# Optimization experiments

Measured on AMD Instinct MI355X. Metric: run time of the kernel, lower is better.

Reference implementation:

```python
import jax, jax.numpy as jnp
import numpy as np

N5, N4, N3, K = 10242, 2562, 642, 7  # icosphere node counts (levels 5,4,3), spatial kernel size
M = 32  # mchannel
EPS = 1e-8


def _sconv(x, neigh, W, b, relu=True):
    # x: [B,T,N,Cin]; neigh: [N,K] 1-ring indices; W: [K,Cin,Cout]
    xn = x[:, :, neigh, :]                        # [B,T,N,K,Cin] irregular gather
    y = jnp.einsum('btnkc,kcd->btnd', xn, W) + b  # per-node kernel contraction
    return jax.nn.relu(y) if relu else y


def _spool(x, pidx):
    # max-pool fine->coarse mesh: pidx [Ncoarse,Kp] indexes fine nodes
    return jnp.max(x[:, :, pidx, :], axis=3)


def _unpool(x, uidx):
    # coarse->fine copy: uidx [Nfine] indexes coarse nodes
    return x[:, :, uidx, :]


def _cos(f, a):
    # torch.nn.CosineSimilarity(dim=-1): dot / max(|f|*|a|, eps)
    dot = jnp.sum(f * a, axis=-1)
    nf = jnp.linalg.norm(f, axis=-1)
    na = jnp.linalg.norm(a, axis=-1)
    return dot / jnp.maximum(nf * na, EPS)


def setup_inputs() -> dict:
    key = jax.random.key(0)
    ks = jax.random.split(key, 32)
    w = lambda i, shape: jax.random.normal(ks[i], shape, jnp.float32) * 0.05
    inp = {
        'frame': jax.random.normal(ks[0], (1, 16, N5, 3), jnp.float32),
        'aem': jax.random.normal(ks[1], (1, 16, N5), jnp.float32),
        'W0f': w(2, (K, 3, M)),        'b0f': w(3, (M,)),
        'W0a': w(4, (K, 1, M)),        'b0a': w(5, (M,)),
        'W1f': w(6, (K, M, 2 * M)),    'b1f': w(7, (2 * M,)),
        'W1a': w(8, (K, M, 2 * M)),    'b1a': w(9, (2 * M,)),
        'W2f': w(10, (K, 2 * M, 4 * M)), 'b2f': w(11, (4 * M,)),
        'W2a': w(12, (K, 2 * M, 4 * M)), 'b2a': w(13, (4 * M,)),
        'W7': w(14, (K, 12 * M, 2 * M)), 'b7': w(15, (2 * M,)),
        'W8': w(16, (K, 4 * M, M)),    'b8': w(17, (M,)),
        'W9': w(18, (K, M, 1)),        'b9': w(19, (1,)),
        'neigh5': jax.random.randint(ks[20], (N5, K), 0, N5),
        'neigh4': jax.random.randint(ks[21], (N4, K), 0, N4),
        'neigh3': jax.random.randint(ks[22], (N3, K), 0, N3),
        'pool5': jax.random.randint(ks[23], (N4, K), 0, N5),
        'pool4': jax.random.randint(ks[24], (N3, K), 0, N4),
        'up4': jax.random.randint(ks[25], (N4,), 0, N3),
        'up5': jax.random.randint(ks[26], (N5,), 0, N4),
        'Tlocation': jax.random.randint(ks[27], (1, 16), 0, 16),
    }
    return inp


def reference(frame, aem, W0f, b0f, W0a, b0a, W1f, b1f, W1a, b1a, W2f, b2f,
              W2a, b2a, W7, b7, W8, b8, W9, b9,
              neigh5, neigh4, neigh3, pool5, pool4, up4, up5, Tlocation):
    a = aem[..., None]                                    # [B,T,N5,1]
    # encoder level 0 (N5)
    c0f = _sconv(frame, neigh5, W0f, b0f)
    c0a = _sconv(a, neigh5, W0a, b0a)
    p0f = _spool(c0f, pool5)
    p0a = _spool(c0a, pool5)
    m0 = _cos(c0f, c0a)[..., None]                        # [B,T,N5,1]
    c0f_att, c0a_att = c0f * m0, c0a * m0
    # encoder level 1 (N4)
    c1f = _sconv(p0f, neigh4, W1f, b1f)
    c1a = _sconv(p0a, neigh4, W1a, b1a)
    p1f = _spool(c1f, pool4)
    p1a = _spool(c1a, pool4)
    m1 = _cos(c1f, c1a)[..., None]
    c1f_att, c1a_att = c1f * m1, c1a * m1
    # bottleneck (N3)
    c2f = _sconv(p1f, neigh3, W2f, b2f)
    c2a = _sconv(p1a, neigh3, W2a, b2a)
    m2 = _cos(c2f, c2a)[..., None]
    conv2 = jnp.concatenate((c2f * m2, c2a * m2), axis=-1)  # [B,T,N3,8M]
    # decoder
    cat7 = jnp.concatenate((_unpool(conv2, up4), c1f_att, c1a_att), axis=-1)  # [B,T,N4,12M]
    conv7 = _sconv(cat7, neigh4, W7, b7)
    cat8 = jnp.concatenate((_unpool(conv7, up5), c0f_att, c0a_att), axis=-1)  # [B,T,N5,4M]
    conv8 = _sconv(cat8, neigh5, W8, b8)
    conv9 = _sconv(conv8, neigh5, W9, b9, relu=False)[..., 0]  # [B,T,N5]
    return jax.nn.softmax(conv9, axis=-1)
```

## Files before the change

### kernel.cpp

```cpp
#include <hip/hip_runtime.h>
#include <cfloat>
#include <cstdint>


constexpr int T  = 16;
constexpr int n5 = 10242, n4 = 2562, n3 = 642;
constexpr int K  = 7;

using bf16x8 = __attribute__((ext_vector_type(8))) short;
using f32x4  = __attribute__((ext_vector_type(4))) float;

static __device__ __forceinline__ float bf2f(unsigned short u) {
    return __uint_as_float((unsigned)u << 16);
}
static __device__ __forceinline__ unsigned short f2bf(float x) {
    unsigned u = __float_as_uint(x);
    u += 0x7FFF + ((u >> 16) & 1);
    return (unsigned short)(u >> 16);
}

__global__ __launch_bounds__(256) void conv0_kernel(
    const float* __restrict__ frame, const float* __restrict__ aem,
    const float* __restrict__ W0f, const float* __restrict__ b0f,
    const float* __restrict__ W0a, const float* __restrict__ b0a,
    const int* __restrict__ neigh5,
    unsigned short* __restrict__ c0f, unsigned short* __restrict__ c0a,
    unsigned short* __restrict__ att0)
{
    const int g = threadIdx.x >> 5;
    const int d = threadIdx.x & 31;
    const int per_t = (n5 + 7) / 8;
    const int t = blockIdx.x / per_t;
    const int n = (blockIdx.x % per_t) * 8 + g;
    if (n >= n5) return;

    float accf = b0f[d];
    float acca = b0a[d];
    const int* nb = neigh5 + n * K;
    #pragma unroll
    for (int k = 0; k < K; ++k) {
        const int j = nb[k];
        const float* fr = frame + ((size_t)t * n5 + j) * 3;
        const float av = aem[(size_t)t * n5 + j];
        accf = fmaf(fr[0], W0f[(k * 3 + 0) * 32 + d], accf);
        accf = fmaf(fr[1], W0f[(k * 3 + 1) * 32 + d], accf);
        accf = fmaf(fr[2], W0f[(k * 3 + 2) * 32 + d], accf);
        acca = fmaf(av, W0a[k * 32 + d], acca);
    }
    accf = fmaxf(accf, 0.f);
    acca = fmaxf(acca, 0.f);

    float dot = accf * acca, ff = accf * accf, aa = acca * acca;
    #pragma unroll
    for (int m = 1; m < 32; m <<= 1) {
        dot += __shfl_xor(dot, m, 32);
        ff  += __shfl_xor(ff,  m, 32);
        aa  += __shfl_xor(aa,  m, 32);
    }
    const float mm = dot / fmaxf(sqrtf(ff) * sqrtf(aa), 1e-8f);
    const size_t base = ((size_t)t * n5 + n) * 32;
    c0f[base + d] = f2bf(accf);
    c0a[base + d] = f2bf(acca);
    const size_t abase = ((size_t)t * n5 + n) * 64;
    att0[abase + d]      = f2bf(accf * mm);
    att0[abase + 32 + d] = f2bf(acca * mm);
}

template<int C>
__global__ __launch_bounds__(256) void pool_kernel(
    const unsigned short* __restrict__ in, const int* __restrict__ pidx,
    int Nin, int Nout, unsigned short* __restrict__ out)
{
    constexpr int C8 = C / 8;
    const int idx = blockIdx.x * 256 + threadIdx.x;
    if (idx >= T * Nout * C8) return;
    const int c8 = idx % C8;
    const int n  = (idx / C8) % Nout;
    const int t  = idx / (C8 * Nout);
    const int* pp = pidx + n * K;
    float m[8];
    #pragma unroll
    for (int j = 0; j < 8; ++j) m[j] = -FLT_MAX;
    #pragma unroll
    for (int k = 0; k < K; ++k) {
        const uint4 v = reinterpret_cast<const uint4*>(in)[((size_t)t * Nin + pp[k]) * C8 + c8];
        const unsigned short* s = reinterpret_cast<const unsigned short*>(&v);
        #pragma unroll
        for (int j = 0; j < 8; ++j) m[j] = fmaxf(m[j], bf2f(s[j]));
    }
    unsigned short o[8];
    #pragma unroll
    for (int j = 0; j < 8; ++j) o[j] = f2bf(m[j]);
    reinterpret_cast<uint4*>(out)[((size_t)t * Nout + n) * C8 + c8] =
        *reinterpret_cast<const uint4*>(o);
}

template<int C, int NN>
__global__ __launch_bounds__(256) void cosatt_kernel(
    const unsigned short* __restrict__ f, const unsigned short* __restrict__ a,
    unsigned short* __restrict__ att)
{
    constexpr int CPL = C / 64;
    const int w = threadIdx.x >> 6, lane = threadIdx.x & 63;
    const int idx = blockIdx.x * 4 + w;
    if (idx >= T * NN) return;
    const unsigned short* fr = f + (size_t)idx * C;
    const unsigned short* ar = a + (size_t)idx * C;
    float xs[CPL], ys[CPL];
    float dot = 0.f, ff = 0.f, aa = 0.f;
    #pragma unroll
    for (int i = 0; i < CPL; ++i) {
        const float x = bf2f(fr[lane + i * 64]);
        const float y = bf2f(ar[lane + i * 64]);
        xs[i] = x; ys[i] = y;
        dot = fmaf(x, y, dot);
        ff  = fmaf(x, x, ff);
        aa  = fmaf(y, y, aa);
    }
    #pragma unroll
    for (int msk = 1; msk < 64; msk <<= 1) {
        dot += __shfl_xor(dot, msk);
        ff  += __shfl_xor(ff,  msk);
        aa  += __shfl_xor(aa,  msk);
    }
    const float m = dot / fmaxf(sqrtf(ff) * sqrtf(aa), 1e-8f);
    unsigned short* orow = att + (size_t)idx * 2 * C;
    #pragma unroll
    for (int i = 0; i < CPL; ++i) {
        orow[lane + i * 64]     = f2bf(xs[i] * m);
        orow[C + lane + i * 64] = f2bf(ys[i] * m);
    }
}

struct PlainB16 {
    const uint4* x; int N; int C8;
    struct Ref { int o; };
    __device__ __forceinline__ Ref prep(int t, int node) const {
        return { (int)(((size_t)t * N + node) * C8) };
    }
    __device__ __forceinline__ uint4 chunk(const Ref& r, int c8) const {
        return x[r.o + c8];
    }
};

struct Cat7B16 {
    const uint4* att2; const uint4* att1; const int* up4;
    __device__ __forceinline__ uint4 row8(int t, int node, int c8) const {
        if (c8 < 32)
            return att2[((size_t)t * n3 + up4[node]) * 32 + c8];
        return att1[((size_t)t * n4 + node) * 16 + (c8 - 32)];
    }
};

struct Cat8B16 {
    const uint4* cv7; const uint4* att0; const int* up5;
    __device__ __forceinline__ uint4 row8(int t, int node, int c8) const {
        if (c8 < 8)
            return cv7[((size_t)t * n4 + up5[node]) * 8 + c8];
        return att0[((size_t)t * n5 + node) * 8 + (c8 - 8)];
    }
};

__global__ __launch_bounds__(256) void wprep_all_kernel(
    const float* __restrict__ W1f, const float* __restrict__ W1a,
    const float* __restrict__ W2f, const float* __restrict__ W2a,
    const float* __restrict__ W7,  const float* __restrict__ W8,
    unsigned short* __restrict__ Wt1f, unsigned short* __restrict__ Wt1a,
    unsigned short* __restrict__ Wt2f, unsigned short* __restrict__ Wt2a,
    unsigned short* __restrict__ Wt7,  unsigned short* __restrict__ Wt8)
{
    int idx = blockIdx.x * 256 + threadIdx.x;
    const float* W; unsigned short* Wt; int KCv, CO;
    if (idx < 14336)       { W = W1f; Wt = Wt1f; KCv = 224;  CO = 64;  }
    else if (idx < 28672)  { idx -= 14336;  W = W1a; Wt = Wt1a; KCv = 224;  CO = 64;  }
    else if (idx < 86016)  { idx -= 28672;  W = W2f; Wt = Wt2f; KCv = 448;  CO = 128; }
    else if (idx < 143360) { idx -= 86016;  W = W2a; Wt = Wt2a; KCv = 448;  CO = 128; }
    else if (idx < 315392) { idx -= 143360; W = W7;  Wt = Wt7;  KCv = 2688; CO = 64;  }
    else                   { idx -= 315392; W = W8;  Wt = Wt8;  KCv = 896;  CO = 32;  }
    const int d = idx / KCv, kc = idx - d * KCv;
    Wt[idx] = f2bf(W[(size_t)kc * CO + d]);
}

template<int CIN, int COUT, int BM, int BN, class Loader>
__global__ __launch_bounds__(256) void gemm_z_kernel(
    Loader ldr, int N, int Mt,
    const unsigned short* __restrict__ Wt,
    unsigned short* __restrict__ Z)
{
    constexpr int KC   = K * CIN;
    constexpr int ND   = K * COUT;
    constexpr int BK   = 64;
    constexpr int KSTEPS = CIN / BK;
    constexpr int U4R  = BK / 8;
    constexpr int WGR_N = BN / 32;
    constexpr int WGR_M = 4 / WGR_N;
    constexpr int DG   = COUT / BN;
    constexpr int NT   = K * DG;
    constexpr int VPTA = BM * U4R / 256;
    constexpr int VPTW = BN * U4R / 256 > 0 ? BN * U4R / 256 : 1;
    static_assert(BM == WGR_M * 32 && CIN % BK == 0 && BN * U4R >= 256);

    __shared__ __align__(16) unsigned short As[BM * BK];
    __shared__ __align__(16) unsigned short Ws[BN * BK];

    const int xcd = blockIdx.x & 7;
    int rest = blockIdx.x >> 3;
    const int half = Mt * NT;
    const int hi = (rest >= half) ? 1 : 0;
    const int t  = 2 * xcd + hi;
    const int j  = rest - hi * half;
    const int tile_m = j / NT;
    const int tnk    = j % NT;
    const int kk_ = tnk / DG;
    const int dg  = tnk % DG;

    const int tid = threadIdx.x, lane = tid & 63, wave = tid >> 6;
    const int wr = wave / WGR_N, wc = wave % WGR_N;
    const int l15 = lane & 15, lhi = lane >> 4;
    const int m0 = tile_m * BM;

    f32x4 acc[2][2] = {};

    for (int ks = 0; ks < KSTEPS; ++ks) {
        uint4 av[VPTA];
        #pragma unroll
        for (int v = 0; v < VPTA; ++v) {
            const int g = tid + v * 256, row = g / U4R, c8 = g % U4R;
            av[v] = ldr.row8(t, min(m0 + row, N - 1), ks * U4R + c8);
        }
        uint4 wv[VPTW];
        #pragma unroll
        for (int v = 0; v < VPTW; ++v) {
            const int g = tid + v * 256, d = g / U4R, c8 = g % U4R;
            wv[v] = *reinterpret_cast<const uint4*>(
                Wt + (size_t)(dg * BN + d) * KC + kk_ * CIN + ks * BK + c8 * 8);
        }

        __syncthreads();
        #pragma unroll
        for (int v = 0; v < VPTA; ++v) {
            const int g = tid + v * 256, row = g / U4R, c8 = g % U4R;
            *reinterpret_cast<uint4*>(&As[(row * BK + c8 * 8) ^ ((row & 7) << 3)]) = av[v];
        }
        #pragma unroll
        for (int v = 0; v < VPTW; ++v) {
            const int g = tid + v * 256, d = g / U4R, c8 = g % U4R;
            *reinterpret_cast<uint4*>(&Ws[(d * BK + c8 * 8) ^ ((d & 7) << 3)]) = wv[v];
        }
        __syncthreads();

        #pragma unroll
        for (int kk2 = 0; kk2 < BK / 32; ++kk2) {
            const int kb = kk2 * 32 + lhi * 8;
            bf16x8 a[2], b[2];
            #pragma unroll
            for (int m = 0; m < 2; ++m) {
                const int row = wr * 32 + m * 16 + l15;
                a[m] = *reinterpret_cast<const bf16x8*>(&As[(row * BK + kb) ^ ((row & 7) << 3)]);
            }
            #pragma unroll
            for (int n = 0; n < 2; ++n) {
                const int col = wc * 32 + n * 16 + l15;
                b[n] = *reinterpret_cast<const bf16x8*>(&Ws[(col * BK + kb) ^ ((col & 7) << 3)]);
            }
            #pragma unroll
            for (int m = 0; m < 2; ++m)
                #pragma unroll
                for (int n = 0; n < 2; ++n)
                    acc[m][n] = __builtin_amdgcn_mfma_f32_16x16x32_bf16(a[m], b[n], acc[m][n], 0, 0, 0);
        }
    }

    const int zc0 = kk_ * COUT + dg * BN;
    #pragma unroll
    for (int n = 0; n < 2; ++n) {
        const int gcol = zc0 + wc * 32 + n * 16 + l15;
        #pragma unroll
        for (int m = 0; m < 2; ++m) {
            #pragma unroll
            for (int i = 0; i < 4; ++i) {
                const int grow = m0 + wr * 32 + m * 16 + lhi * 4 + i;
                if (grow < N)
                    Z[((size_t)t * N + grow) * ND + gcol] = f2bf(acc[m][n][i]);
            }
        }
    }
}

template<int COUT>
__global__ __launch_bounds__(256) void epi_reduce_kernel(
    const unsigned short* __restrict__ Z, const int* __restrict__ neigh, int N,
    const float* __restrict__ bias, unsigned short* __restrict__ out)
{
    constexpr int ND = K * COUT;
    constexpr int C8 = COUT / 8;
    const int idx = blockIdx.x * 256 + threadIdx.x;
    if (idx >= T * N * C8) return;
    const int c8 = idx % C8;
    const int n  = (idx / C8) % N;
    const int t  = idx / (C8 * N);
    const int* nb = neigh + n * K;

    float s[8];
    #pragma unroll
    for (int j = 0; j < 8; ++j) s[j] = bias[c8 * 8 + j];
    #pragma unroll
    for (int k = 0; k < K; ++k) {
        const uint4 v = *reinterpret_cast<const uint4*>(
            &Z[((size_t)t * N + nb[k]) * ND + k * COUT + c8 * 8]);
        const unsigned short* p = reinterpret_cast<const unsigned short*>(&v);
        #pragma unroll
        for (int j = 0; j < 8; ++j) s[j] += bf2f(p[j]);
    }
    unsigned short o[8];
    #pragma unroll
    for (int j = 0; j < 8; ++j) o[j] = f2bf(fmaxf(s[j], 0.f));
    *reinterpret_cast<uint4*>(&out[((size_t)t * N + n) * COUT + c8 * 8]) =
        *reinterpret_cast<const uint4*>(o);
}

template<int CIN, int COUT, class Loader>
__device__ __forceinline__ void sconv_tile(
    const Loader& ldr, const int* __restrict__ neigh, int N, int t,
    int tile_m, int tile_n,
    const unsigned short* __restrict__ Wt, const float* __restrict__ bias,
    unsigned short* __restrict__ out)
{
    constexpr int KC     = K * CIN;
    constexpr int CHUNKS = CIN / 32;
    constexpr int STEPS  = K * CHUNKS;
    constexpr int D      = STEPS < 3 ? STEPS : 3;

    const int lane = threadIdx.x & 63;
    const int l15 = lane & 15, lhi = lane >> 4;

    const int r0 = tile_m * 32 + l15;
    const int row0 = min(r0, N - 1), row1 = min(r0 + 16, N - 1);

    typename Loader::Ref ref0[K], ref1[K];
    #pragma unroll
    for (int k = 0; k < K; ++k) {
        ref0[k] = ldr.prep(t, neigh[row0 * K + k]);
        ref1[k] = ldr.prep(t, neigh[row1 * K + k]);
    }

    const int col0 = tile_n * 32 + l15;
    const unsigned short* w0p = Wt + (size_t)col0 * KC + lhi * 8;
    const unsigned short* w1p = w0p + (size_t)16 * KC;

    uint4 qa0[D], qa1[D], qb0[D], qb1[D];

    auto issue = [&](int s, int slot) {
        const int k = s / CHUNKS, c = s - k * CHUNKS;
        const int c8 = c * 4 + lhi;
        qa0[slot] = ldr.chunk(ref0[k], c8);
        qa1[slot] = ldr.chunk(ref1[k], c8);
        qb0[slot] = *reinterpret_cast<const uint4*>(w0p + k * CIN + c * 32);
        qb1[slot] = *reinterpret_cast<const uint4*>(w1p + k * CIN + c * 32);
    };

    f32x4 acc[2][2] = {};

    #pragma unroll
    for (int s = 0; s < D; ++s) issue(s, s);
    __builtin_amdgcn_sched_barrier(0);

    #pragma unroll
    for (int s = 0; s < STEPS; ++s) {
        const int slot = s % D;
        const bf16x8 a0 = __builtin_bit_cast(bf16x8, qa0[slot]);
        const bf16x8 a1 = __builtin_bit_cast(bf16x8, qa1[slot]);
        const bf16x8 b0 = __builtin_bit_cast(bf16x8, qb0[slot]);
        const bf16x8 b1 = __builtin_bit_cast(bf16x8, qb1[slot]);
        acc[0][0] = __builtin_amdgcn_mfma_f32_16x16x32_bf16(a0, b0, acc[0][0], 0, 0, 0);
        acc[0][1] = __builtin_amdgcn_mfma_f32_16x16x32_bf16(a0, b1, acc[0][1], 0, 0, 0);
        acc[1][0] = __builtin_amdgcn_mfma_f32_16x16x32_bf16(a1, b0, acc[1][0], 0, 0, 0);
        acc[1][1] = __builtin_amdgcn_mfma_f32_16x16x32_bf16(a1, b1, acc[1][1], 0, 0, 0);
        if (s + D < STEPS) issue(s + D, slot);
        __builtin_amdgcn_sched_barrier(0);
    }

    #pragma unroll
    for (int n = 0; n < 2; ++n) {
        const int gcol = tile_n * 32 + n * 16 + l15;
        const float bv = bias[gcol];
        #pragma unroll
        for (int m = 0; m < 2; ++m) {
            #pragma unroll
            for (int i = 0; i < 4; ++i) {
                const int grow = tile_m * 32 + m * 16 + lhi * 4 + i;
                if (grow < N)
                    out[((size_t)t * N + grow) * COUT + gcol] =
                        f2bf(fmaxf(acc[m][n][i] + bv, 0.f));
            }
        }
    }
}

template<int CIN, int COUT, class Loader>
__global__ __launch_bounds__(64, 2) void sconv_rd2_kernel(
    Loader lf, Loader la, const int* __restrict__ neigh, int N, int U,
    const unsigned short* __restrict__ Wtf, const unsigned short* __restrict__ Wta,
    const float* __restrict__ bf_, const float* __restrict__ ba_,
    unsigned short* __restrict__ of_, unsigned short* __restrict__ oa_)
{
    constexpr int TN = COUT / 32;
    const int xcd = blockIdx.x & 7;
    int idx = blockIdx.x >> 3;
    const int sel = idx & 1; idx >>= 1;
    const int hi = (idx >= U) ? 1 : 0;
    const int t  = 2 * xcd + hi;
    const int w  = idx - hi * U;
    const Loader L = sel ? la : lf;
    const unsigned short* Wt = sel ? Wta : Wtf;
    const float* bias = sel ? ba_ : bf_;
    unsigned short* out = sel ? oa_ : of_;
    sconv_tile<CIN, COUT, Loader>(L, neigh, N, t, w / TN, w % TN, Wt, bias, out);
}

__global__ __launch_bounds__(256) void conv9_kernel(
    const unsigned short* __restrict__ cv8, const int* __restrict__ neigh5,
    const float* __restrict__ W9, const float* __restrict__ b9,
    float* __restrict__ logits)
{
    const int idx = blockIdx.x * 256 + threadIdx.x;
    if (idx >= T * n5) return;
    const int n = idx % n5;
    const int t = idx / n5;
    float acc = b9[0];
    const int* nb = neigh5 + n * K;
    #pragma unroll
    for (int k = 0; k < K; ++k) {
        const uint4* row = reinterpret_cast<const uint4*>(cv8 + ((size_t)t * n5 + nb[k]) * 32);
        const float* wk = W9 + k * 32;
        #pragma unroll
        for (int c4 = 0; c4 < 4; ++c4) {
            const uint4 v = row[c4];
            const unsigned short* s = reinterpret_cast<const unsigned short*>(&v);
            #pragma unroll
            for (int jj = 0; jj < 8; ++jj)
                acc = fmaf(bf2f(s[jj]), wk[c4 * 8 + jj], acc);
        }
    }
    logits[idx] = acc;
}

__global__ __launch_bounds__(1024) void softmax_kernel(
    const float* __restrict__ logits, float* __restrict__ out)
{
    const int t = blockIdx.x, tid = threadIdx.x;
    const float* x = logits + (size_t)t * n5;
    float* y = out + (size_t)t * n5;
    __shared__ float redmax[16], redsum[16];

    float mx = -FLT_MAX;
    for (int i = tid; i < n5; i += 1024) mx = fmaxf(mx, x[i]);
    #pragma unroll
    for (int m = 1; m < 64; m <<= 1) mx = fmaxf(mx, __shfl_xor(mx, m));
    if ((tid & 63) == 0) redmax[tid >> 6] = mx;
    __syncthreads();
    mx = redmax[0];
    #pragma unroll
    for (int i = 1; i < 16; ++i) mx = fmaxf(mx, redmax[i]);

    float s = 0.f;
    for (int i = tid; i < n5; i += 1024) s += expf(x[i] - mx);
    #pragma unroll
    for (int m = 1; m < 64; m <<= 1) s += __shfl_xor(s, m);
    if ((tid & 63) == 0) redsum[tid >> 6] = s;
    __syncthreads();
    s = 0.f;
    #pragma unroll
    for (int i = 0; i < 16; ++i) s += redsum[i];

    for (int i = tid; i < n5; i += 1024) y[i] = expf(x[i] - mx) / s;
}

extern "C" void kernel_launch(void* const* d_in, const int* in_sizes, int n_in,
                              void* d_out, int out_size, void* d_ws, size_t ws_size,
                              hipStream_t stream)
{
    const float* frame = (const float*)d_in[0];
    const float* aem   = (const float*)d_in[1];
    const float* W0f = (const float*)d_in[2];
    const float* b0f = (const float*)d_in[3];
    const float* W0a = (const float*)d_in[4];
    const float* b0a = (const float*)d_in[5];
    const float* W1f = (const float*)d_in[6];
    const float* b1f = (const float*)d_in[7];
    const float* W1a = (const float*)d_in[8];
    const float* b1a = (const float*)d_in[9];
    const float* W2f = (const float*)d_in[10];
    const float* b2f = (const float*)d_in[11];
    const float* W2a = (const float*)d_in[12];
    const float* b2a = (const float*)d_in[13];
    const float* W7  = (const float*)d_in[14];
    const float* b7  = (const float*)d_in[15];
    const float* W8  = (const float*)d_in[16];
    const float* b8  = (const float*)d_in[17];
    const float* W9  = (const float*)d_in[18];
    const float* b9  = (const float*)d_in[19];
    const int* neigh5 = (const int*)d_in[20];
    const int* neigh4 = (const int*)d_in[21];
    const int* neigh3 = (const int*)d_in[22];
    const int* pool5  = (const int*)d_in[23];
    const int* pool4  = (const int*)d_in[24];
    const int* up4    = (const int*)d_in[25];
    const int* up5    = (const int*)d_in[26];

    unsigned short* wsu = (unsigned short*)d_ws;
    size_t off = 0;
    auto ua = [&](size_t n) {
        unsigned short* p = wsu + off; off += (n + 7) & ~(size_t)7; return p;
    };
    unsigned short* c0f  = ua((size_t)T * n5 * 32);
    unsigned short* c0a  = ua((size_t)T * n5 * 32);
    unsigned short* att0 = ua((size_t)T * n5 * 64);
    unsigned short* p0f  = ua((size_t)T * n4 * 32);
    unsigned short* p0a  = ua((size_t)T * n4 * 32);
    unsigned short* c1f  = ua((size_t)T * n4 * 64);
    unsigned short* c1a  = ua((size_t)T * n4 * 64);
    unsigned short* att1 = ua((size_t)T * n4 * 128);
    unsigned short* p1f  = ua((size_t)T * n3 * 64);
    unsigned short* p1a  = ua((size_t)T * n3 * 64);
    unsigned short* c2f  = ua((size_t)T * n3 * 128);
    unsigned short* c2a  = ua((size_t)T * n3 * 128);
    unsigned short* att2 = ua((size_t)T * n3 * 256);
    unsigned short* cv7  = ua((size_t)T * n4 * 64);
    unsigned short* cv8  = ua((size_t)T * n5 * 32);
    unsigned short* Wt1f = ua((size_t)64 * 224);
    unsigned short* Wt1a = ua((size_t)64 * 224);
    unsigned short* Wt2f = ua((size_t)128 * 448);
    unsigned short* Wt2a = ua((size_t)128 * 448);
    unsigned short* Wt7  = ua((size_t)64 * 2688);
    unsigned short* Wt8  = ua((size_t)32 * 896);
    unsigned short* Zbuf = ua((size_t)T * n5 * 224);
    float* lgt = (float*)(wsu + ((off + 1) & ~(size_t)1));

    wprep_all_kernel<<<1344, 256, 0, stream>>>(
        W1f, W1a, W2f, W2a, W7, W8, Wt1f, Wt1a, Wt2f, Wt2a, Wt7, Wt8);

    conv0_kernel<<<T * ((n5 + 7) / 8), 256, 0, stream>>>(
        frame, aem, W0f, b0f, W0a, b0a, neigh5, c0f, c0a, att0);

    {
        const int thr = T * n4 * (32 / 8);
        pool_kernel<32><<<(thr + 255) / 256, 256, 0, stream>>>(c0f, pool5, n5, n4, p0f);
        pool_kernel<32><<<(thr + 255) / 256, 256, 0, stream>>>(c0a, pool5, n5, n4, p0a);
    }

    {
        constexpr int U = 81 * 2;
        sconv_rd2_kernel<32, 64><<<8 * 4 * U, 64, 0, stream>>>(
            PlainB16{(const uint4*)p0f, n4, 4}, PlainB16{(const uint4*)p0a, n4, 4},
            neigh4, n4, U, Wt1f, Wt1a, b1f, b1a, c1f, c1a);
    }
    cosatt_kernel<64, n4><<<(T * n4 + 3) / 4, 256, 0, stream>>>(c1f, c1a, att1);

    {
        const int thr = T * n3 * (64 / 8);
        pool_kernel<64><<<(thr + 255) / 256, 256, 0, stream>>>(c1f, pool4, n4, n3, p1f);
        pool_kernel<64><<<(thr + 255) / 256, 256, 0, stream>>>(c1a, pool4, n4, n3, p1a);
    }

    {
        constexpr int U = 21 * 4;
        sconv_rd2_kernel<64, 128><<<8 * 4 * U, 64, 0, stream>>>(
            PlainB16{(const uint4*)p1f, n3, 8}, PlainB16{(const uint4*)p1a, n3, 8},
            neigh3, n3, U, Wt2f, Wt2a, b2f, b2a, c2f, c2a);
    }
    cosatt_kernel<128, n3><<<(T * n3 + 3) / 4, 256, 0, stream>>>(c2f, c2a, att2);

    {
        constexpr int Mt = (n4 + 63) / 64;
        gemm_z_kernel<384, 64, 64, 64><<<16 * Mt * 7, 256, 0, stream>>>(
            Cat7B16{(const uint4*)att2, (const uint4*)att1, up4}, n4, Mt, Wt7, Zbuf);
        const int thr = T * n4 * 8;
        epi_reduce_kernel<64><<<(thr + 255) / 256, 256, 0, stream>>>(
            Zbuf, neigh4, n4, b7, cv7);
    }

    {
        constexpr int Mt = (n5 + 127) / 128;
        gemm_z_kernel<128, 32, 128, 32><<<16 * Mt * 7, 256, 0, stream>>>(
            Cat8B16{(const uint4*)cv7, (const uint4*)att0, up5}, n5, Mt, Wt8, Zbuf);
        const int thr = T * n5 * 4;
        epi_reduce_kernel<32><<<(thr + 255) / 256, 256, 0, stream>>>(
            Zbuf, neigh5, n5, b8, cv8);
    }

    conv9_kernel<<<(T * n5 + 255) / 256, 256, 0, stream>>>(cv8, neigh5, W9, b9, lgt);

    softmax_kernel<<<T, 1024, 0, stream>>>(lgt, (float*)d_out);
}
```

Baseline: 279.1 us.

## Split decoder GEMMs to apply unpooled weights at coarse resolution

The decoder convolutions now run the weight contraction for the unpooled (coarse) channel block at the coarse mesh resolution instead of on the unpooled fine rows. Conv7 computes att2 rows at N3 and conv8 computes cv7 rows at N4. A dual epilogue then gathers through the unpool index per neighbour and sums both partial products. This cuts the GEMM work for the upsampled channels and simplifies the loaders into plain strided GEMMs with LDS-staged coalesced output stores, at the cost of an extra indirection and a second Z read in the epilogue.

```diff
diff --git a/kernel.cpp b/kernel.cpp
--- a/kernel.cpp
+++ b/kernel.cpp
@@ -143,81 +143,72 @@
     }
 };
 
-struct Cat7B16 {
-    const uint4* att2; const uint4* att1; const int* up4;
-    __device__ __forceinline__ uint4 row8(int t, int node, int c8) const {
-        if (c8 < 32)
-            return att2[((size_t)t * n3 + up4[node]) * 32 + c8];
-        return att1[((size_t)t * n4 + node) * 16 + (c8 - 32)];
-    }
-};
-
-struct Cat8B16 {
-    const uint4* cv7; const uint4* att0; const int* up5;
-    __device__ __forceinline__ uint4 row8(int t, int node, int c8) const {
-        if (c8 < 8)
-            return cv7[((size_t)t * n4 + up5[node]) * 8 + c8];
-        return att0[((size_t)t * n5 + node) * 8 + (c8 - 8)];
-    }
-};
-
 __global__ __launch_bounds__(256) void wprep_all_kernel(
     const float* __restrict__ W1f, const float* __restrict__ W1a,
     const float* __restrict__ W2f, const float* __restrict__ W2a,
     const float* __restrict__ W7,  const float* __restrict__ W8,
     unsigned short* __restrict__ Wt1f, unsigned short* __restrict__ Wt1a,
     unsigned short* __restrict__ Wt2f, unsigned short* __restrict__ Wt2a,
-    unsigned short* __restrict__ Wt7,  unsigned short* __restrict__ Wt8)
+    unsigned short* __restrict__ Wt7a, unsigned short* __restrict__ Wt7b,
+    unsigned short* __restrict__ Wt8a, unsigned short* __restrict__ Wt8b)
 {
     int idx = blockIdx.x * 256 + threadIdx.x;
-    const float* W; unsigned short* Wt; int KCv, CO;
-    if (idx < 14336)       { W = W1f; Wt = Wt1f; KCv = 224;  CO = 64;  }
-    else if (idx < 28672)  { idx -= 14336;  W = W1a; Wt = Wt1a; KCv = 224;  CO = 64;  }
-    else if (idx < 86016)  { idx -= 28672;  W = W2f; Wt = Wt2f; KCv = 448;  CO = 128; }
-    else if (idx < 143360) { idx -= 86016;  W = W2a; Wt = Wt2a; KCv = 448;  CO = 128; }
-    else if (idx < 315392) { idx -= 143360; W = W7;  Wt = Wt7;  KCv = 2688; CO = 64;  }
-    else                   { idx -= 315392; W = W8;  Wt = Wt8;  KCv = 896;  CO = 32;  }
-    const int d = idx / KCv, kc = idx - d * KCv;
-    Wt[idx] = f2bf(W[(size_t)kc * CO + d]);
-}
-
-template<int CIN, int COUT, int BM, int BN, class Loader>
-__global__ __launch_bounds__(256) void gemm_z_kernel(
-    Loader ldr, int N, int Mt,
+    if (idx < 143360) {
+        const float* W; unsigned short* Wt; int KCv, CO;
+        if (idx < 14336)       { W = W1f; Wt = Wt1f; KCv = 224;  CO = 64;  }
+        else if (idx < 28672)  { idx -= 14336; W = W1a; Wt = Wt1a; KCv = 224; CO = 64; }
+        else if (idx < 86016)  { idx -= 28672; W = W2f; Wt = Wt2f; KCv = 448; CO = 128; }
+        else                   { idx -= 86016; W = W2a; Wt = Wt2a; KCv = 448; CO = 128; }
+        const int d = idx / KCv, kc = idx - d * KCv;
+        Wt[idx] = f2bf(W[(size_t)kc * CO + d]);
+    } else if (idx < 258048) {
+        const int l = idx - 143360;
+        const int kd = l >> 8, c = l & 255;
+        const int k = kd >> 6, d = kd & 63;
+        Wt7a[l] = f2bf(W7[((size_t)k * 384 + c) * 64 + d]);
+    } else if (idx < 315392) {
+        const int l = idx - 258048;
+        const int kd = l >> 7, c = l & 127;
+        const int k = kd >> 6, d = kd & 63;
+        Wt7b[l] = f2bf(W7[((size_t)k * 384 + 256 + c) * 64 + d]);
+    } else if (idx < 329728) {
+        const int l = idx - 315392;
+        const int kd = l >> 6, c = l & 63;
+        const int k = kd >> 5, d = kd & 31;
+        Wt8a[l] = f2bf(W8[((size_t)k * 128 + c) * 32 + d]);
+    } else if (idx < 344064) {
+        const int l = idx - 329728;
+        const int kd = l >> 6, c = l & 63;
+        const int k = kd >> 5, d = kd & 31;
+        Wt8b[l] = f2bf(W8[((size_t)k * 128 + 64 + c) * 32 + d]);
+    }
+}
+
+template<int CINs, int NDIM, int BM, int BN>
+__global__ __launch_bounds__(256) void gemm_c_kernel(
+    const unsigned short* __restrict__ A, int M,
     const unsigned short* __restrict__ Wt,
     unsigned short* __restrict__ Z)
 {
-    constexpr int KC   = K * CIN;
-    constexpr int ND   = K * COUT;
-    constexpr int BK   = 64;
-    constexpr int KSTEPS = CIN / BK;
-    constexpr int U4R  = BK / 8;
+    constexpr int KSTEPS = CINs / 64;
+    constexpr int NT    = NDIM / BN;
+    constexpr int U4R   = 8;
     constexpr int WGR_N = BN / 32;
     constexpr int WGR_M = 4 / WGR_N;
-    constexpr int DG   = COUT / BN;
-    constexpr int NT   = K * DG;
-    constexpr int VPTA = BM * U4R / 256;
-    constexpr int VPTW = BN * U4R / 256 > 0 ? BN * U4R / 256 : 1;
-    static_assert(BM == WGR_M * 32 && CIN % BK == 0 && BN * U4R >= 256);
-
-    __shared__ __align__(16) unsigned short As[BM * BK];
-    __shared__ __align__(16) unsigned short Ws[BN * BK];
-
-    const int xcd = blockIdx.x & 7;
-    int rest = blockIdx.x >> 3;
-    const int half = Mt * NT;
-    const int hi = (rest >= half) ? 1 : 0;
-    const int t  = 2 * xcd + hi;
-    const int j  = rest - hi * half;
-    const int tile_m = j / NT;
-    const int tnk    = j % NT;
-    const int kk_ = tnk / DG;
-    const int dg  = tnk % DG;
+    constexpr int VPTA  = BM * U4R / 256;
+    constexpr int VPTW  = BN * U4R / 256;
+    static_assert(BM == WGR_M * 32 && CINs % 64 == 0 && VPTW >= 1);
+
+    __shared__ __align__(16) unsigned short As[BM * 64];
+    __shared__ __align__(16) unsigned short Ws[BN * 64];
+
+    const int tile_m = blockIdx.x / NT;
+    const int tile_n = blockIdx.x % NT;
+    const int m0 = tile_m * BM;
 
     const int tid = threadIdx.x, lane = tid & 63, wave = tid >> 6;
     const int wr = wave / WGR_N, wc = wave % WGR_N;
     const int l15 = lane & 15, lhi = lane >> 4;
-    const int m0 = tile_m * BM;
 
     f32x4 acc[2][2] = {};
 
@@ -225,43 +216,44 @@
         uint4 av[VPTA];
         #pragma unroll
         for (int v = 0; v < VPTA; ++v) {
-            const int g = tid + v * 256, row = g / U4R, c8 = g % U4R;
-            av[v] = ldr.row8(t, min(m0 + row, N - 1), ks * U4R + c8);
+            const int g = tid + v * 256, row = g >> 3, c8 = g & 7;
+            av[v] = *reinterpret_cast<const uint4*>(
+                A + (size_t)min(m0 + row, M - 1) * CINs + ks * 64 + c8 * 8);
         }
         uint4 wv[VPTW];
         #pragma unroll
         for (int v = 0; v < VPTW; ++v) {
-            const int g = tid + v * 256, d = g / U4R, c8 = g % U4R;
+            const int g = tid + v * 256, d = g >> 3, c8 = g & 7;
             wv[v] = *reinterpret_cast<const uint4*>(
-                Wt + (size_t)(dg * BN + d) * KC + kk_ * CIN + ks * BK + c8 * 8);
+                Wt + (size_t)(tile_n * BN + d) * CINs + ks * 64 + c8 * 8);
         }
 
         __syncthreads();
         #pragma unroll
         for (int v = 0; v < VPTA; ++v) {
-            const int g = tid + v * 256, row = g / U4R, c8 = g % U4R;
-            *reinterpret_cast<uint4*>(&As[(row * BK + c8 * 8) ^ ((row & 7) << 3)]) = av[v];
+            const int g = tid + v * 256, row = g >> 3, c8 = g & 7;
+            *reinterpret_cast<uint4*>(&As[(row * 64 + c8 * 8) ^ ((row & 7) << 3)]) = av[v];
         }
         #pragma unroll
         for (int v = 0; v < VPTW; ++v) {
-            const int g = tid + v * 256, d = g / U4R, c8 = g % U4R;
-            *reinterpret_cast<uint4*>(&Ws[(d * BK + c8 * 8) ^ ((d & 7) << 3)]) = wv[v];
+            const int g = tid + v * 256, d = g >> 3, c8 = g & 7;
+            *reinterpret_cast<uint4*>(&Ws[(d * 64 + c8 * 8) ^ ((d & 7) << 3)]) = wv[v];
         }
         __syncthreads();
 
         #pragma unroll
-        for (int kk2 = 0; kk2 < BK / 32; ++kk2) {
+        for (int kk2 = 0; kk2 < 2; ++kk2) {
             const int kb = kk2 * 32 + lhi * 8;
             bf16x8 a[2], b[2];
             #pragma unroll
             for (int m = 0; m < 2; ++m) {
                 const int row = wr * 32 + m * 16 + l15;
-                a[m] = *reinterpret_cast<const bf16x8*>(&As[(row * BK + kb) ^ ((row & 7) << 3)]);
+                a[m] = *reinterpret_cast<const bf16x8*>(&As[(row * 64 + kb) ^ ((row & 7) << 3)]);
             }
             #pragma unroll
             for (int n = 0; n < 2; ++n) {
                 const int col = wc * 32 + n * 16 + l15;
-                b[n] = *reinterpret_cast<const bf16x8*>(&Ws[(col * BK + kb) ^ ((col & 7) << 3)]);
+                b[n] = *reinterpret_cast<const bf16x8*>(&Ws[(col * 64 + kb) ^ ((col & 7) << 3)]);
             }
             #pragma unroll
             for (int m = 0; m < 2; ++m)
@@ -271,26 +263,35 @@
         }
     }
 
-    const int zc0 = kk_ * COUT + dg * BN;
+    __syncthreads();
+    unsigned short* Cs = As;
     #pragma unroll
     for (int n = 0; n < 2; ++n) {
-        const int gcol = zc0 + wc * 32 + n * 16 + l15;
-        #pragma unroll
-        for (int m = 0; m < 2; ++m) {
+        const int col = wc * 32 + n * 16 + l15;
+        #pragma unroll
+        for (int m = 0; m < 2; ++m)
             #pragma unroll
-            for (int i = 0; i < 4; ++i) {
-                const int grow = m0 + wr * 32 + m * 16 + lhi * 4 + i;
-                if (grow < N)
-                    Z[((size_t)t * N + grow) * ND + gcol] = f2bf(acc[m][n][i]);
-            }
-        }
+            for (int i = 0; i < 4; ++i)
+                Cs[(wr * 32 + m * 16 + lhi * 4 + i) * BN + col] = f2bf(acc[m][n][i]);
+    }
+    __syncthreads();
+    constexpr int RPT = BN / 8;
+    constexpr int CV  = BM * BN / 8 / 256;
+    #pragma unroll
+    for (int v = 0; v < CV; ++v) {
+        const int g = tid + v * 256, row = g / RPT, c8 = g % RPT;
+        const int grow = m0 + row;
+        if (grow < M)
+            *reinterpret_cast<uint4*>(&Z[(size_t)grow * NDIM + tile_n * BN + c8 * 8]) =
+                *reinterpret_cast<const uint4*>(&Cs[row * BN + c8 * 8]);
     }
 }
 
 template<int COUT>
-__global__ __launch_bounds__(256) void epi_reduce_kernel(
-    const unsigned short* __restrict__ Z, const int* __restrict__ neigh, int N,
-    const float* __restrict__ bias, unsigned short* __restrict__ out)
+__global__ __launch_bounds__(256) void epi_dual_kernel(
+    const unsigned short* __restrict__ Zu, const unsigned short* __restrict__ Zb,
+    const int* __restrict__ up, const int* __restrict__ neigh,
+    int N, int Nu, const float* __restrict__ bias, unsigned short* __restrict__ out)
 {
     constexpr int ND = K * COUT;
     constexpr int C8 = COUT / 8;
@@ -306,11 +307,16 @@
     for (int j = 0; j < 8; ++j) s[j] = bias[c8 * 8 + j];
     #pragma unroll
     for (int k = 0; k < K; ++k) {
-        const uint4 v = *reinterpret_cast<const uint4*>(
-            &Z[((size_t)t * N + nb[k]) * ND + k * COUT + c8 * 8]);
-        const unsigned short* p = reinterpret_cast<const unsigned short*>(&v);
-        #pragma unroll
-        for (int j = 0; j < 8; ++j) s[j] += bf2f(p[j]);
+        const int jn = nb[k];
+        const int ju = up[jn];
+        const uint4 vu = *reinterpret_cast<const uint4*>(
+            &Zu[((size_t)t * Nu + ju) * ND + k * COUT + c8 * 8]);
+        const uint4 vb = *reinterpret_cast<const uint4*>(
+            &Zb[((size_t)t * N + jn) * ND + k * COUT + c8 * 8]);
+        const unsigned short* pu = reinterpret_cast<const unsigned short*>(&vu);
+        const unsigned short* pb = reinterpret_cast<const unsigned short*>(&vb);
+        #pragma unroll
+        for (int j = 0; j < 8; ++j) s[j] += bf2f(pu[j]) + bf2f(pb[j]);
     }
     unsigned short o[8];
     #pragma unroll
@@ -532,13 +538,20 @@
     unsigned short* Wt1a = ua((size_t)64 * 224);
     unsigned short* Wt2f = ua((size_t)128 * 448);
     unsigned short* Wt2a = ua((size_t)128 * 448);
-    unsigned short* Wt7  = ua((size_t)64 * 2688);
-    unsigned short* Wt8  = ua((size_t)32 * 896);
-    unsigned short* Zbuf = ua((size_t)T * n5 * 224);
+    unsigned short* Wt7a = ua((size_t)448 * 256);
+    unsigned short* Wt7b = ua((size_t)448 * 128);
+    unsigned short* Wt8a = ua((size_t)224 * 64);
+    unsigned short* Wt8b = ua((size_t)224 * 64);
+    unsigned short* arena = ua((size_t)T * n4 * 224 + (size_t)T * n5 * 224);
+    unsigned short* Z2  = arena;
+    unsigned short* Zb7 = arena + (size_t)T * n3 * 448;
+    unsigned short* Z7s = arena;
+    unsigned short* Zb8 = arena + (size_t)T * n4 * 224;
     float* lgt = (float*)(wsu + ((off + 1) & ~(size_t)1));
 
     wprep_all_kernel<<<1344, 256, 0, stream>>>(
-        W1f, W1a, W2f, W2a, W7, W8, Wt1f, Wt1a, Wt2f, Wt2a, Wt7, Wt8);
+        W1f, W1a, W2f, W2a, W7, W8,
+        Wt1f, Wt1a, Wt2f, Wt2a, Wt7a, Wt7b, Wt8a, Wt8b);
 
     conv0_kernel<<<T * ((n5 + 7) / 8), 256, 0, stream>>>(
         frame, aem, W0f, b0f, W0a, b0a, neigh5, c0f, c0a, att0);
@@ -572,21 +585,27 @@
     cosatt_kernel<128, n3><<<(T * n3 + 3) / 4, 256, 0, stream>>>(c2f, c2a, att2);
 
     {
-        constexpr int Mt = (n4 + 63) / 64;
-        gemm_z_kernel<384, 64, 64, 64><<<16 * Mt * 7, 256, 0, stream>>>(
-            Cat7B16{(const uint4*)att2, (const uint4*)att1, up4}, n4, Mt, Wt7, Zbuf);
+        constexpr int M2 = T * n3;
+        constexpr int Mb = T * n4;
+        gemm_c_kernel<256, 448, 64, 64><<<((M2 + 63) / 64) * 7, 256, 0, stream>>>(
+            att2, M2, Wt7a, Z2);
+        gemm_c_kernel<128, 448, 64, 64><<<((Mb + 63) / 64) * 7, 256, 0, stream>>>(
+            att1, Mb, Wt7b, Zb7);
         const int thr = T * n4 * 8;
-        epi_reduce_kernel<64><<<(thr + 255) / 256, 256, 0, stream>>>(
-            Zbuf, neigh4, n4, b7, cv7);
+        epi_dual_kernel<64><<<(thr + 255) / 256, 256, 0, stream>>>(
+            Z2, Zb7, up4, neigh4, n4, n3, b7, cv7);
     }
 
     {
-        constexpr int Mt = (n5 + 127) / 128;
-        gemm_z_kernel<128, 32, 128, 32><<<16 * Mt * 7, 256, 0, stream>>>(
-            Cat8B16{(const uint4*)cv7, (const uint4*)att0, up5}, n5, Mt, Wt8, Zbuf);
+        constexpr int Ms = T * n4;
+        constexpr int Mb = T * n5;
+        gemm_c_kernel<64, 224, 128, 32><<<((Ms + 127) / 128) * 7, 256, 0, stream>>>(
+            cv7, Ms, Wt8a, Z7s);
+        gemm_c_kernel<64, 224, 128, 32><<<((Mb + 127) / 128) * 7, 256, 0, stream>>>(
+            att0, Mb, Wt8b, Zb8);
         const int thr = T * n5 * 4;
-        epi_reduce_kernel<32><<<(thr + 255) / 256, 256, 0, stream>>>(
-            Zbuf, neigh5, n5, b8, cv8);
+        epi_dual_kernel<32><<<(thr + 255) / 256, 256, 0, stream>>>(
+            Z7s, Zb8, up5, neigh5, n5, n4, b8, cv8);
     }
 
     conv9_kernel<<<(T * n5 + 255) / 256, 256, 0, stream>>>(cv8, neigh5, W9, b9, lgt);
```

After: 366.5 us. 31.3% more time.

## Store GEMM partials as per-tap planes with LDS-staged coalesced writes

Applied to the files above, without the earlier changes.

The Z intermediate for the decoder convs moves from an interleaved [t,n,K*COUT] layout to per-tap planes [k,t,n,COUT]. Each GEMM block stages its tile through LDS and writes it as 16-byte vectors instead of scattered 2-byte stores. The reduce kernel is remapped so each XCD handles the same timesteps as the GEMM, aiming for L2 locality. Workspace alignment also rises to 64 elements. This adds an extra LDS round trip and a barrier per block.

```diff
diff --git a/kernel.cpp b/kernel.cpp
--- a/kernel.cpp
+++ b/kernel.cpp
@@ -181,38 +181,33 @@
     Wt[idx] = f2bf(W[(size_t)kc * CO + d]);
 }
 
-template<int CIN, int COUT, int BM, int BN, class Loader>
-__global__ __launch_bounds__(256) void gemm_z_kernel(
+template<int CIN, int COUT, int BM, class Loader>
+__global__ __launch_bounds__(256) void gemm_zp_kernel(
     Loader ldr, int N, int Mt,
     const unsigned short* __restrict__ Wt,
     unsigned short* __restrict__ Z)
 {
-    constexpr int KC   = K * CIN;
-    constexpr int ND   = K * COUT;
-    constexpr int BK   = 64;
+    constexpr int KC    = K * CIN;
+    constexpr int BK    = 64;
     constexpr int KSTEPS = CIN / BK;
-    constexpr int U4R  = BK / 8;
-    constexpr int WGR_N = BN / 32;
+    constexpr int U4R   = BK / 8;
+    constexpr int WGR_N = COUT / 32;
     constexpr int WGR_M = 4 / WGR_N;
-    constexpr int DG   = COUT / BN;
-    constexpr int NT   = K * DG;
-    constexpr int VPTA = BM * U4R / 256;
-    constexpr int VPTW = BN * U4R / 256 > 0 ? BN * U4R / 256 : 1;
-    static_assert(BM == WGR_M * 32 && CIN % BK == 0 && BN * U4R >= 256);
+    constexpr int VPTA  = BM * U4R / 256;
+    constexpr int VPTW  = COUT * U4R / 256;
+    static_assert(BM == WGR_M * 32 && CIN % BK == 0 && VPTW >= 1 && BM * COUT <= BM * BK);
 
     __shared__ __align__(16) unsigned short As[BM * BK];
-    __shared__ __align__(16) unsigned short Ws[BN * BK];
+    __shared__ __align__(16) unsigned short Ws[COUT * BK];
 
     const int xcd = blockIdx.x & 7;
     int rest = blockIdx.x >> 3;
-    const int half = Mt * NT;
+    const int half = Mt * K;
     const int hi = (rest >= half) ? 1 : 0;
     const int t  = 2 * xcd + hi;
     const int j  = rest - hi * half;
-    const int tile_m = j / NT;
-    const int tnk    = j % NT;
-    const int kk_ = tnk / DG;
-    const int dg  = tnk % DG;
+    const int tile_m = j / K;
+    const int kk_    = j % K;
 
     const int tid = threadIdx.x, lane = tid & 63, wave = tid >> 6;
     const int wr = wave / WGR_N, wc = wave % WGR_N;
@@ -233,7 +228,7 @@
         for (int v = 0; v < VPTW; ++v) {
             const int g = tid + v * 256, d = g / U4R, c8 = g % U4R;
             wv[v] = *reinterpret_cast<const uint4*>(
-                Wt + (size_t)(dg * BN + d) * KC + kk_ * CIN + ks * BK + c8 * 8);
+                Wt + (size_t)d * KC + kk_ * CIN + ks * BK + c8 * 8);
         }
 
         __syncthreads();
@@ -250,7 +245,7 @@
         __syncthreads();
 
         #pragma unroll
-        for (int kk2 = 0; kk2 < BK / 32; ++kk2) {
+        for (int kk2 = 0; kk2 < 2; ++kk2) {
             const int kb = kk2 * 32 + lhi * 8;
             bf16x8 a[2], b[2];
             #pragma unroll
@@ -271,34 +266,45 @@
         }
     }
 
-    const int zc0 = kk_ * COUT + dg * BN;
+    __syncthreads();
+    unsigned short* Cs = As;
     #pragma unroll
     for (int n = 0; n < 2; ++n) {
-        const int gcol = zc0 + wc * 32 + n * 16 + l15;
-        #pragma unroll
-        for (int m = 0; m < 2; ++m) {
+        const int col = wc * 32 + n * 16 + l15;
+        #pragma unroll
+        for (int m = 0; m < 2; ++m)
             #pragma unroll
-            for (int i = 0; i < 4; ++i) {
-                const int grow = m0 + wr * 32 + m * 16 + lhi * 4 + i;
-                if (grow < N)
-                    Z[((size_t)t * N + grow) * ND + gcol] = f2bf(acc[m][n][i]);
-            }
-        }
+            for (int i = 0; i < 4; ++i)
+                Cs[(wr * 32 + m * 16 + lhi * 4 + i) * COUT + col] = f2bf(acc[m][n][i]);
+    }
+    __syncthreads();
+    constexpr int RPT = COUT / 8;
+    constexpr int CV  = BM * COUT / 8 / 256;
+    #pragma unroll
+    for (int v = 0; v < CV; ++v) {
+        const int g = tid + v * 256, row = g / RPT, c8 = g % RPT;
+        const int grow = m0 + row;
+        if (grow < N)
+            *reinterpret_cast<uint4*>(
+                &Z[(((size_t)kk_ * T + t) * N + grow) * COUT + c8 * 8]) =
+                *reinterpret_cast<const uint4*>(&Cs[row * COUT + c8 * 8]);
     }
 }
 
 template<int COUT>
-__global__ __launch_bounds__(256) void epi_reduce_kernel(
-    const unsigned short* __restrict__ Z, const int* __restrict__ neigh, int N,
-    const float* __restrict__ bias, unsigned short* __restrict__ out)
-{
-    constexpr int ND = K * COUT;
+__global__ __launch_bounds__(256) void epi_p_kernel(
+    const unsigned short* __restrict__ Z, const int* __restrict__ neigh,
+    int N, int Bt, const float* __restrict__ bias, unsigned short* __restrict__ out)
+{
     constexpr int C8 = COUT / 8;
-    const int idx = blockIdx.x * 256 + threadIdx.x;
-    if (idx >= T * N * C8) return;
-    const int c8 = idx % C8;
-    const int n  = (idx / C8) % N;
-    const int t  = idx / (C8 * N);
+    const int xcd = blockIdx.x & 7;
+    int idx = blockIdx.x >> 3;
+    const int hi = (idx >= Bt) ? 1 : 0;
+    const int t  = 2 * xcd + hi;
+    const int e  = (idx - hi * Bt) * 256 + threadIdx.x;
+    if (e >= N * C8) return;
+    const int c8 = e % C8;
+    const int n  = e / C8;
     const int* nb = neigh + n * K;
 
     float s[8];
@@ -307,7 +313,7 @@
     #pragma unroll
     for (int k = 0; k < K; ++k) {
         const uint4 v = *reinterpret_cast<const uint4*>(
-            &Z[((size_t)t * N + nb[k]) * ND + k * COUT + c8 * 8]);
+            &Z[(((size_t)k * T + t) * N + nb[k]) * COUT + c8 * 8]);
         const unsigned short* p = reinterpret_cast<const unsigned short*>(&v);
         #pragma unroll
         for (int j = 0; j < 8; ++j) s[j] += bf2f(p[j]);
@@ -511,7 +517,7 @@
     unsigned short* wsu = (unsigned short*)d_ws;
     size_t off = 0;
     auto ua = [&](size_t n) {
-        unsigned short* p = wsu + off; off += (n + 7) & ~(size_t)7; return p;
+        unsigned short* p = wsu + off; off += (n + 63) & ~(size_t)63; return p;
     };
     unsigned short* c0f  = ua((size_t)T * n5 * 32);
     unsigned short* c0a  = ua((size_t)T * n5 * 32);
@@ -534,7 +540,7 @@
     unsigned short* Wt2a = ua((size_t)128 * 448);
     unsigned short* Wt7  = ua((size_t)64 * 2688);
     unsigned short* Wt8  = ua((size_t)32 * 896);
-    unsigned short* Zbuf = ua((size_t)T * n5 * 224);
+    unsigned short* Zbuf = ua((size_t)K * T * n5 * 32);
     float* lgt = (float*)(wsu + ((off + 1) & ~(size_t)1));
 
     wprep_all_kernel<<<1344, 256, 0, stream>>>(
@@ -573,20 +579,20 @@
 
     {
         constexpr int Mt = (n4 + 63) / 64;
-        gemm_z_kernel<384, 64, 64, 64><<<16 * Mt * 7, 256, 0, stream>>>(
+        gemm_zp_kernel<384, 64, 64><<<16 * Mt * K, 256, 0, stream>>>(
             Cat7B16{(const uint4*)att2, (const uint4*)att1, up4}, n4, Mt, Wt7, Zbuf);
-        const int thr = T * n4 * 8;
-        epi_reduce_kernel<64><<<(thr + 255) / 256, 256, 0, stream>>>(
-            Zbuf, neigh4, n4, b7, cv7);
+        constexpr int Bt = (n4 * 8 + 255) / 256;
+        epi_p_kernel<64><<<8 * 2 * Bt, 256, 0, stream>>>(
+            Zbuf, neigh4, n4, Bt, b7, cv7);
     }
 
     {
         constexpr int Mt = (n5 + 127) / 128;
-        gemm_z_kernel<128, 32, 128, 32><<<16 * Mt * 7, 256, 0, stream>>>(
+        gemm_zp_kernel<128, 32, 128><<<16 * Mt * K, 256, 0, stream>>>(
             Cat8B16{(const uint4*)cv7, (const uint4*)att0, up5}, n5, Mt, Wt8, Zbuf);
-        const int thr = T * n5 * 4;
-        epi_reduce_kernel<32><<<(thr + 255) / 256, 256, 0, stream>>>(
-            Zbuf, neigh5, n5, b8, cv8);
+        constexpr int Bt = (n5 * 4 + 255) / 256;
+        epi_p_kernel<32><<<8 * 2 * Bt, 256, 0, stream>>>(
+            Zbuf, neigh5, n5, Bt, b8, cv8);
     }
 
     conv9_kernel<<<(T * n5 + 255) / 256, 256, 0, stream>>>(cv8, neigh5, W9, b9, lgt);
```

Result: faster. 265.4 us (median of 2 runs) (-4.9%).
